# Kernel tuning notes

Hardware: AMD Instinct MI355X
Metric: run time of the kernel (lower is better)

Reference implementation:

```python
import jax, jax.numpy as jnp
import numpy as np

N_NODES = 50000
IN, H, OUT = 128, 256, 128  # in_channels, hidden_channels, out_channels
E, PE = 640000, 500000
EPS = 1e-5


def setup_inputs() -> dict:
    key = jax.random.key(0)
    ks = jax.random.split(key, 12)
    def rn(k, shape, s=0.05):
        return jax.random.normal(k, shape, jnp.float32) * s
    return {
        "x": jax.random.normal(ks[0], (N_NODES, IN), jnp.float32),
        "edge_index": jax.random.randint(ks[1], (2, E), 0, N_NODES, jnp.int32),
        "pred_edge_index": jax.random.randint(ks[2], (2, PE), 0, N_NODES, jnp.int32),
        # SAGEConv 1: out = mean_neighbors @ W_l^T + x @ W_r^T + b (PyG default, root_weight=True)
        "W1l": rn(ks[3], (H, IN)), "W1r": rn(ks[4], (H, IN)), "b1": jnp.zeros((H,), jnp.float32),
        "bn1_g": jnp.ones((H,), jnp.float32), "bn1_b": jnp.zeros((H,), jnp.float32),
        "bn1_m": jnp.zeros((H,), jnp.float32), "bn1_v": jnp.ones((H,), jnp.float32),
        # SAGEConv 2
        "W2l": rn(ks[5], (OUT, H)), "W2r": rn(ks[6], (OUT, H)), "b2": jnp.zeros((OUT,), jnp.float32),
        # LinkPredictor MLP
        "pW1": rn(ks[7], (H, 2 * OUT)), "pb1": jnp.zeros((H,), jnp.float32),
        "pbn1_g": jnp.ones((H,), jnp.float32), "pbn1_b": jnp.zeros((H,), jnp.float32),
        "pbn1_m": jnp.zeros((H,), jnp.float32), "pbn1_v": jnp.ones((H,), jnp.float32),
        "pW2": rn(ks[8], (H // 2, H)), "pb2": jnp.zeros((H // 2,), jnp.float32),
        "pbn2_g": jnp.ones((H // 2,), jnp.float32), "pbn2_b": jnp.zeros((H // 2,), jnp.float32),
        "pbn2_m": jnp.zeros((H // 2,), jnp.float32), "pbn2_v": jnp.ones((H // 2,), jnp.float32),
        "pW3": rn(ks[9], (1, H // 2)), "pb3": jnp.zeros((1,), jnp.float32),
    }


def _bn(x, g, b, m, v):
    # BatchNorm1d in eval mode (running stats)
    return (x - m) * jax.lax.rsqrt(v + EPS) * g + b


def _sage(x, src, dst, Wl, Wr, b):
    # mean aggregation of source features onto targets (gather-scatter)
    agg = jax.ops.segment_sum(x[src], dst, num_segments=N_NODES)
    cnt = jax.ops.segment_sum(jnp.ones(src.shape, x.dtype), dst, num_segments=N_NODES)
    mean = agg / jnp.maximum(cnt, 1.0)[:, None]
    return mean @ Wl.T + x @ Wr.T + b


def reference(x, edge_index, pred_edge_index, W1l, W1r, b1, bn1_g, bn1_b, bn1_m, bn1_v,
              W2l, W2r, b2, pW1, pb1, pbn1_g, pbn1_b, pbn1_m, pbn1_v,
              pW2, pb2, pbn2_g, pbn2_b, pbn2_m, pbn2_v, pW3, pb3):
    src, dst = edge_index[0], edge_index[1]
    # encoder (dropout is identity in eval mode)
    h = _sage(x, src, dst, W1l, W1r, b1)
    h = jax.nn.relu(_bn(h, bn1_g, bn1_b, bn1_m, bn1_v))
    z = _sage(h, src, dst, W2l, W2r, b2)  # [N_NODES, OUT]
    # decoder: gather endpoint embeddings and run MLP
    q = jnp.concatenate([z[pred_edge_index[0]], z[pred_edge_index[1]]], axis=-1)  # [PE, 2*OUT]
    q = jax.nn.relu(_bn(q @ pW1.T + pb1, pbn1_g, pbn1_b, pbn1_m, pbn1_v))
    q = jax.nn.relu(_bn(q @ pW2.T + pb2, pbn2_g, pbn2_b, pbn2_m, pbn2_v))
    return (q @ pW3.T + pb3).squeeze(-1)  # [PE]
```

## Files before the change

kernel.cpp:

```cpp
#include <hip/hip_runtime.h>
#include <hip/hip_bf16.h>

#define NN   50000
#define NE   640000
#define NPE  500000
#define FEPS 1e-5f

typedef __attribute__((ext_vector_type(8))) short          bf16x8;
typedef __attribute__((ext_vector_type(8))) unsigned short u16x8;
typedef __attribute__((ext_vector_type(4))) float          f32x4;

__device__ inline float b2f(unsigned short u) {
    union { unsigned int i; float f; } c; c.i = (unsigned int)u << 16; return c.f;
}
__device__ inline unsigned short f2b(float f) {
    __hip_bfloat16 h = __float2bfloat16(f);
    return *reinterpret_cast<unsigned short*>(&h);
}

__global__ __launch_bounds__(256) void k_init(
    int4* __restrict__ zdst,
    const float* __restrict__ x, unsigned short* __restrict__ xbf,
    const float* __restrict__ W1l, const float* __restrict__ W1r,
    const float* __restrict__ W2l, const float* __restrict__ W2r,
    const float* __restrict__ pW1, const float* __restrict__ pW2,
    unsigned short* __restrict__ wdst) {
    int b = blockIdx.x, t = threadIdx.x;
    if (b < 196) {
        int i = b * 256 + t;
        if (i < 50048) zdst[i] = make_int4(0, 0, 0, 0);
        return;
    }
    const float* src;
    size_t off;
    if (b < 3321) {
        int i = (b - 196) * 256 + t;
        if (i >= 800000) return;
        const float4* p = (const float4*)x + 2 * (size_t)i;
        float4 a = p[0], c = p[1];
        u16x8 o;
        o[0]=f2b(a.x); o[1]=f2b(a.y); o[2]=f2b(a.z); o[3]=f2b(a.w);
        o[4]=f2b(c.x); o[5]=f2b(c.y); o[6]=f2b(c.z); o[7]=f2b(c.w);
        *((u16x8*)xbf + i) = o;
        return;
    }
    int i = (b - 3321) * 256 + t;
    if (i >= 28672) return;
    if      (i < 4096)  { src = W1l; off = i; }
    else if (i < 8192)  { src = W1r; off = i - 4096; }
    else if (i < 12288) { src = W2l; off = i - 8192; }
    else if (i < 16384) { src = W2r; off = i - 12288; }
    else if (i < 24576) { src = pW1; off = i - 16384; }
    else                { src = pW2; off = i - 24576; }
    const float4* p = (const float4*)src + 2 * off;
    float4 a = p[0], c = p[1];
    u16x8 o;
    o[0]=f2b(a.x); o[1]=f2b(a.y); o[2]=f2b(a.z); o[3]=f2b(a.w);
    o[4]=f2b(c.x); o[5]=f2b(c.y); o[6]=f2b(c.z); o[7]=f2b(c.w);
    *((u16x8*)wdst + i) = o;
}

__global__ void k_hist(const int* __restrict__ key, int* __restrict__ cnt, int n) {
    int e = blockIdx.x * blockDim.x + threadIdx.x;
    if (e < n) atomicAdd(&cnt[key[e]], 1);
}

__global__ void k_scan1(const int* __restrict__ cnt, int* __restrict__ part) {
    int t = threadIdx.x, lane = t & 63, w = t >> 6;
    int i = blockIdx.x * 256 + t;
    int v = (i < NN) ? cnt[i] : 0;
#pragma unroll
    for (int d = 1; d < 64; d <<= 1) v += __shfl_xor(v, d, 64);
    __shared__ int ws[4];
    if (lane == 0) ws[w] = v;
    __syncthreads();
    if (t == 0) part[blockIdx.x] = ws[0] + ws[1] + ws[2] + ws[3];
}

__global__ void k_scan2(int* __restrict__ part) {
    int t = threadIdx.x, lane = t & 63, w = t >> 6;
    int v = (t < 196) ? part[t] : 0;
    int s = v;
#pragma unroll
    for (int d = 1; d < 64; d <<= 1) { int u = __shfl_up(s, d, 64); if (lane >= d) s += u; }
    __shared__ int ws[4];
    if (lane == 63) ws[w] = s;
    __syncthreads();
    if (t == 0) { int a = 0; for (int k = 0; k < 4; ++k) { int tmp = ws[k]; ws[k] = a; a += tmp; } }
    __syncthreads();
    if (t < 196) part[t] = ws[w] + s - v;
}

__global__ void k_scan3(const int* __restrict__ cnt, const int* __restrict__ part,
                        int* __restrict__ rowptr) {
    int t = threadIdx.x, lane = t & 63, w = t >> 6;
    int i = blockIdx.x * 256 + t;
    int v = (i < NN) ? cnt[i] : 0;
    int s = v;
#pragma unroll
    for (int d = 1; d < 64; d <<= 1) { int u = __shfl_up(s, d, 64); if (lane >= d) s += u; }
    __shared__ int ws[4];
    if (lane == 63) ws[w] = s;
    __syncthreads();
    if (t == 0) { int a = 0; for (int k = 0; k < 4; ++k) { int tmp = ws[k]; ws[k] = a; a += tmp; } }
    __syncthreads();
    if (i <= NN) rowptr[i] = part[blockIdx.x] + ws[w] + s - v;
}

__global__ void k_fill(const int* __restrict__ src, const int* __restrict__ dst,
                       const int* __restrict__ rowptr, int* __restrict__ cursor,
                       int* __restrict__ col) {
    int e = blockIdx.x * blockDim.x + threadIdx.x;
    if (e >= NE) return;
    int d = dst[e];
    int slot = atomicAdd(&cursor[d], 1);
    col[rowptr[d] + slot] = src[e];
}

__global__ void k_fill2(const int* __restrict__ pu, const int* __restrict__ pv,
                        const int* __restrict__ rowptr2, int* __restrict__ cursor2,
                        int* __restrict__ su, int2* __restrict__ svi) {
    int e = blockIdx.x * blockDim.x + threadIdx.x;
    if (e >= NPE) return;
    int u = pu[e];
    int slot = atomicAdd(&cursor2[u], 1);
    int pos = rowptr2[u] + slot;
    su[pos] = u;
    svi[pos] = make_int2(pv[e], e);
}

__global__ __launch_bounds__(256) void k_mean(const unsigned short* __restrict__ feat,
                                              const int* __restrict__ rowptr,
                                              const int* __restrict__ col,
                                              unsigned short* __restrict__ outm) {
    int node = blockIdx.x * 4 + (threadIdx.x >> 6);
    int lane = threadIdx.x & 63;
    if (node >= NN) return;
    int beg = rowptr[node], end = rowptr[node + 1];
    float a0 = 0.f, a1 = 0.f;
    int j = beg;
    for (; j + 8 <= end; j += 8) {
        int s[8];
#pragma unroll
        for (int k = 0; k < 8; ++k) s[k] = col[j + k];
        unsigned int v[8];
#pragma unroll
        for (int k = 0; k < 8; ++k)
            v[k] = *(const unsigned int*)(feat + (size_t)s[k] * 128 + lane * 2);
#pragma unroll
        for (int k = 0; k < 8; ++k) { a0 += b2f(v[k] & 0xffff); a1 += b2f(v[k] >> 16); }
    }
    if (j + 4 <= end) {
        int s[4];
#pragma unroll
        for (int k = 0; k < 4; ++k) s[k] = col[j + k];
        unsigned int v[4];
#pragma unroll
        for (int k = 0; k < 4; ++k)
            v[k] = *(const unsigned int*)(feat + (size_t)s[k] * 128 + lane * 2);
#pragma unroll
        for (int k = 0; k < 4; ++k) { a0 += b2f(v[k] & 0xffff); a1 += b2f(v[k] >> 16); }
        j += 4;
    }
    for (; j < end; ++j) {
        int s = col[j];
        unsigned int v = *(const unsigned int*)(feat + (size_t)s * 128 + lane * 2);
        a0 += b2f(v & 0xffff); a1 += b2f(v >> 16);
    }
    float inv = 1.f / fmaxf((float)(end - beg), 1.f);
    unsigned int v = (unsigned int)f2b(a0 * inv) | ((unsigned int)f2b(a1 * inv) << 16);
    *(unsigned int*)(outm + (size_t)node * 128 + lane * 2) = v;
}

__global__ __launch_bounds__(256) void k_sage12(
    const unsigned short* __restrict__ mean, const unsigned short* __restrict__ self,
    const unsigned short* __restrict__ Wl, const unsigned short* __restrict__ Wr,
    const float* __restrict__ b, const float* __restrict__ bg, const float* __restrict__ bb,
    const float* __restrict__ bm, const float* __restrict__ bv,
    const unsigned short* __restrict__ W2l, const unsigned short* __restrict__ W2r,
    const float* __restrict__ b2,
    unsigned short* __restrict__ Y, unsigned short* __restrict__ S) {
    __shared__ unsigned short AB[64 * 256];
    unsigned short* ms = AB;
    unsigned short* xs = AB + 64 * 128;
    int t = threadIdx.x;
    int n0 = blockIdx.x * 64;
    for (int j = 0; j < 4; ++j) {
        int idx = t + j * 256;
        int row = idx >> 4, c16 = idx & 15;
        int node = n0 + row;
        u16x8 v = {0,0,0,0,0,0,0,0}, v2 = {0,0,0,0,0,0,0,0};
        if (node < NN) {
            v  = *(const u16x8*)(mean + (size_t)node * 128 + c16 * 8);
            v2 = *(const u16x8*)(self + (size_t)node * 128 + c16 * 8);
        }
        int byte = row * 256 + ((c16 * 16) ^ ((row & 7) << 4));
        *(u16x8*)((char*)ms + byte) = v;
        *(u16x8*)((char*)xs + byte) = v2;
    }
    __syncthreads();
    int w = t >> 6, l = t & 63, lr = l & 15, lh = l >> 4;
    f32x4 acc[4][4];
#pragma unroll
    for (int mi = 0; mi < 4; ++mi)
#pragma unroll
        for (int ni = 0; ni < 4; ++ni) { acc[mi][ni][0]=0; acc[mi][ni][1]=0; acc[mi][ni][2]=0; acc[mi][ni][3]=0; }
#pragma unroll
    for (int half = 0; half < 2; ++half) {
        const unsigned short* A = half ? xs : ms;
        const unsigned short* W = half ? Wr : Wl;
#pragma unroll
        for (int ks = 0; ks < 4; ++ks) {
            int k0 = ks * 32;
            bf16x8 a[4], wf[4];
#pragma unroll
            for (int mi = 0; mi < 4; ++mi) {
                int row = mi * 16 + lr;
                int byte = row * 256 + ((k0 * 2 + lh * 16) ^ ((row & 7) << 4));
                a[mi] = *(const bf16x8*)((const char*)A + byte);
            }
#pragma unroll
            for (int ni = 0; ni < 4; ++ni) {
                int wrow = w * 64 + ni * 16 + lr;
                wf[ni] = *(const bf16x8*)(W + (size_t)wrow * 128 + k0 + lh * 8);
            }
#pragma unroll
            for (int mi = 0; mi < 4; ++mi)
#pragma unroll
                for (int ni = 0; ni < 4; ++ni)
                    acc[mi][ni] = __builtin_amdgcn_mfma_f32_16x16x32_bf16(a[mi], wf[ni], acc[mi][ni], 0, 0, 0);
        }
    }
    __syncthreads();
#pragma unroll
    for (int ni = 0; ni < 4; ++ni) {
        int ch = w * 64 + ni * 16 + lr;
        float sc = bg[ch] * rsqrtf(bv[ch] + FEPS);
        float sh = bb[ch] - bm[ch] * sc;
        float bias = b[ch];
#pragma unroll
        for (int mi = 0; mi < 4; ++mi)
#pragma unroll
            for (int r = 0; r < 4; ++r) {
                int row = mi * 16 + lh * 4 + r;
                float vv = fmaxf((acc[mi][ni][r] + bias) * sc + sh, 0.f);
                int byte = row * 512 + ((ch * 2) ^ ((row & 7) << 4));
                *(unsigned short*)((char*)AB + byte) = f2b(vv);
            }
    }
    __syncthreads();
    f32x4 aY[4][2], aS[4][2];
#pragma unroll
    for (int mi = 0; mi < 4; ++mi)
#pragma unroll
        for (int ni = 0; ni < 2; ++ni) {
            aY[mi][ni][0]=0; aY[mi][ni][1]=0; aY[mi][ni][2]=0; aY[mi][ni][3]=0;
            aS[mi][ni][0]=0; aS[mi][ni][1]=0; aS[mi][ni][2]=0; aS[mi][ni][3]=0;
        }
#pragma unroll
    for (int ks = 0; ks < 8; ++ks) {
        int k0 = ks * 32;
        bf16x8 a[4], wl[2], wr[2];
#pragma unroll
        for (int mi = 0; mi < 4; ++mi) {
            int row = mi * 16 + lr;
            int byte = row * 512 + ((k0 * 2 + lh * 16) ^ ((row & 7) << 4));
            a[mi] = *(const bf16x8*)((const char*)AB + byte);
        }
#pragma unroll
        for (int ni = 0; ni < 2; ++ni) {
            int wrow = w * 32 + ni * 16 + lr;
            wl[ni] = *(const bf16x8*)(W2l + (size_t)wrow * 256 + k0 + lh * 8);
            wr[ni] = *(const bf16x8*)(W2r + (size_t)wrow * 256 + k0 + lh * 8);
        }
#pragma unroll
        for (int mi = 0; mi < 4; ++mi)
#pragma unroll
            for (int ni = 0; ni < 2; ++ni) {
                aY[mi][ni] = __builtin_amdgcn_mfma_f32_16x16x32_bf16(a[mi], wl[ni], aY[mi][ni], 0, 0, 0);
                aS[mi][ni] = __builtin_amdgcn_mfma_f32_16x16x32_bf16(a[mi], wr[ni], aS[mi][ni], 0, 0, 0);
            }
    }
#pragma unroll
    for (int ni = 0; ni < 2; ++ni) {
        int ch = w * 32 + ni * 16 + lr;
        float bias = b2[ch];
#pragma unroll
        for (int mi = 0; mi < 4; ++mi)
#pragma unroll
            for (int r = 0; r < 4; ++r) {
                int node = n0 + mi * 16 + lh * 4 + r;
                if (node < NN) {
                    Y[(size_t)node * 128 + ch] = f2b(aY[mi][ni][r]);
                    S[(size_t)node * 128 + ch] = f2b(aS[mi][ni][r] + bias);
                }
            }
    }
}

__global__ __launch_bounds__(256) void k_prep(
    const unsigned short* __restrict__ S,
    const unsigned short* __restrict__ mY,
    const unsigned short* __restrict__ W1,
    const float* __restrict__ b1, const float* __restrict__ g1,
    const float* __restrict__ be1, const float* __restrict__ m1, const float* __restrict__ v1,
    unsigned short* __restrict__ Pa, unsigned short* __restrict__ Pb) {
    __shared__ unsigned short zs[64 * 128];
    int t = threadIdx.x;
    int tile = blockIdx.x >> 1, side = blockIdx.x & 1;
    int n0 = tile * 64;
    for (int j = 0; j < 4; ++j) {
        int idx = t + j * 256;
        int row = idx >> 4, c16 = idx & 15;
        int node = n0 + row;
        u16x8 o = {0,0,0,0,0,0,0,0};
        if (node < NN) {
            u16x8 sv = *(const u16x8*)(S  + (size_t)node * 128 + c16 * 8);
            u16x8 mv = *(const u16x8*)(mY + (size_t)node * 128 + c16 * 8);
#pragma unroll
            for (int jj = 0; jj < 8; ++jj)
                o[jj] = f2b(b2f((unsigned short)sv[jj]) + b2f((unsigned short)mv[jj]));
        }
        int byte = row * 256 + ((c16 * 16) ^ ((row & 7) << 4));
        *(u16x8*)((char*)zs + byte) = o;
    }
    __syncthreads();
    int w = t >> 6, l = t & 63, lr = l & 15, lh = l >> 4;
    f32x4 acc[4][4];
#pragma unroll
    for (int mi = 0; mi < 4; ++mi)
#pragma unroll
        for (int ni = 0; ni < 4; ++ni) { acc[mi][ni][0]=0; acc[mi][ni][1]=0; acc[mi][ni][2]=0; acc[mi][ni][3]=0; }
#pragma unroll
    for (int ks = 0; ks < 4; ++ks) {
        int k0 = ks * 32;
        bf16x8 a[4], wf[4];
#pragma unroll
        for (int mi = 0; mi < 4; ++mi) {
            int row = mi * 16 + lr;
            int byte = row * 256 + ((k0 * 2 + lh * 16) ^ ((row & 7) << 4));
            a[mi] = *(const bf16x8*)((const char*)zs + byte);
        }
#pragma unroll
        for (int ni = 0; ni < 4; ++ni) {
            int ch = w * 64 + ni * 16 + lr;
            wf[ni] = *(const bf16x8*)(W1 + (size_t)ch * 256 + side * 128 + k0 + lh * 8);
        }
#pragma unroll
        for (int mi = 0; mi < 4; ++mi)
#pragma unroll
            for (int ni = 0; ni < 4; ++ni)
                acc[mi][ni] = __builtin_amdgcn_mfma_f32_16x16x32_bf16(a[mi], wf[ni], acc[mi][ni], 0, 0, 0);
    }
    unsigned short* P = side ? Pb : Pa;
#pragma unroll
    for (int ni = 0; ni < 4; ++ni) {
        int ch = w * 64 + ni * 16 + lr;
        float sc = g1[ch] * rsqrtf(v1[ch] + FEPS);
        float add = side ? 0.f : ((b1[ch] - m1[ch]) * sc + be1[ch]);
#pragma unroll
        for (int mi = 0; mi < 4; ++mi)
#pragma unroll
            for (int r = 0; r < 4; ++r) {
                int node = n0 + mi * 16 + lh * 4 + r;
                if (node < NN)
                    P[(size_t)node * 256 + ch] = f2b(acc[mi][ni][r] * sc + add);
            }
    }
}

__global__ __launch_bounds__(256, 5) void k_mlp(
    const unsigned short* __restrict__ Pa, const unsigned short* __restrict__ Pb,
    const int* __restrict__ su, const int2* __restrict__ svi,
    const unsigned short* __restrict__ W2, const float* __restrict__ b2,
    const float* __restrict__ g2, const float* __restrict__ be2,
    const float* __restrict__ m2, const float* __restrict__ v2,
    const float* __restrict__ W3, const float* __restrict__ b3,
    float* __restrict__ out) {
    __shared__ unsigned short q1[64 * 256];
    int t = threadIdx.x;
    const int q = 976, r = 5;
    int bid = blockIdx.x;
    int xcd = bid & 7, ii = bid >> 3;
    int wg = (xcd < r) ? (xcd * (q + 1) + ii) : (r * (q + 1) + (xcd - r) * q + ii);
    int e0 = wg * 64;
#pragma unroll
    for (int batch = 0; batch < 2; ++batch) {
        u16x8 A[4], B[4];
        int bofs[4];
#pragma unroll
        for (int j = 0; j < 4; ++j) {
            int idx = t + (batch * 4 + j) * 256;
            int edge = idx >> 5, c16 = idx & 31;
            int ge = e0 + edge;
            if (ge < NPE) {
                int u = su[ge];
                int2 vi = svi[ge];
                A[j] = *(const u16x8*)(Pa + (size_t)u    * 256 + c16 * 8);
                B[j] = *(const u16x8*)(Pb + (size_t)vi.x * 256 + c16 * 8);
            } else {
                A[j] = (u16x8){0,0,0,0,0,0,0,0};
                B[j] = (u16x8){0,0,0,0,0,0,0,0};
            }
            bofs[j] = edge * 512 + ((c16 * 16) ^ ((edge & 7) << 4));
        }
#pragma unroll
        for (int j = 0; j < 4; ++j) {
            u16x8 o;
#pragma unroll
            for (int jj = 0; jj < 8; ++jj)
                o[jj] = f2b(fmaxf(b2f((unsigned short)A[j][jj]) + b2f((unsigned short)B[j][jj]), 0.f));
            *(u16x8*)((char*)q1 + bofs[j]) = o;
        }
    }
    __syncthreads();
    int w = t >> 6, l = t & 63, lr = l & 15, lh = l >> 4;
    f32x4 acc[4][2];
#pragma unroll
    for (int mi = 0; mi < 4; ++mi)
#pragma unroll
        for (int ni = 0; ni < 2; ++ni) { acc[mi][ni][0]=0; acc[mi][ni][1]=0; acc[mi][ni][2]=0; acc[mi][ni][3]=0; }
#pragma unroll
    for (int ks = 0; ks < 8; ++ks) {
        int k0 = ks * 32;
        bf16x8 a[4], wf[2];
#pragma unroll
        for (int mi = 0; mi < 4; ++mi) {
            int row = mi * 16 + lr;
            int byte = row * 512 + ((k0 * 2 + lh * 16) ^ ((row & 7) << 4));
            a[mi] = *(const bf16x8*)((const char*)q1 + byte);
        }
#pragma unroll
        for (int ni = 0; ni < 2; ++ni) {
            int wrow = w * 32 + ni * 16 + lr;
            wf[ni] = *(const bf16x8*)(W2 + (size_t)wrow * 256 + k0 + lh * 8);
        }
#pragma unroll
        for (int mi = 0; mi < 4; ++mi)
#pragma unroll
            for (int ni = 0; ni < 2; ++ni)
                acc[mi][ni] = __builtin_amdgcn_mfma_f32_16x16x32_bf16(a[mi], wf[ni], acc[mi][ni], 0, 0, 0);
    }
    __syncthreads();
#pragma unroll
    for (int ni = 0; ni < 2; ++ni) {
        int ch = w * 32 + ni * 16 + lr;
        float sc = g2[ch] * rsqrtf(v2[ch] + FEPS);
        float sh = be2[ch] - m2[ch] * sc;
        float bias = b2[ch];
#pragma unroll
        for (int mi = 0; mi < 4; ++mi)
#pragma unroll
            for (int r = 0; r < 4; ++r) {
                int row = mi * 16 + lh * 4 + r;
                float vv = fmaxf((acc[mi][ni][r] + bias) * sc + sh, 0.f);
                int byte = row * 256 + ((ch * 2) ^ ((row & 7) << 4));
                *(unsigned short*)((char*)q1 + byte) = f2b(vv);
            }
    }
    __syncthreads();
    {
        int edge = t >> 2, part = t & 3;
        float p = 0.f;
#pragma unroll
        for (int s = 0; s < 4; ++s) {
            int byte = edge * 256 + ((part * 64 + s * 16) ^ ((edge & 7) << 4));
            u16x8 v = *(const u16x8*)((const char*)q1 + byte);
#pragma unroll
            for (int jj = 0; jj < 8; ++jj)
                p += b2f((unsigned short)v[jj]) * W3[part * 32 + s * 8 + jj];
        }
        p += __shfl_xor(p, 1, 64);
        p += __shfl_xor(p, 2, 64);
        int ge = e0 + edge;
        if (part == 0 && ge < NPE) out[svi[ge].y] = p + b3[0];
    }
}

extern "C" void kernel_launch(void* const* d_in, const int* in_sizes, int n_in,
                              void* d_out, int out_size, void* d_ws, size_t ws_size,
                              hipStream_t stream) {
    const float* x    = (const float*)d_in[0];
    const int*   ei   = (const int*)d_in[1];
    const int*   pei  = (const int*)d_in[2];
    const float* W1l  = (const float*)d_in[3];
    const float* W1r  = (const float*)d_in[4];
    const float* b1   = (const float*)d_in[5];
    const float* bn1g = (const float*)d_in[6];
    const float* bn1b = (const float*)d_in[7];
    const float* bn1m = (const float*)d_in[8];
    const float* bn1v = (const float*)d_in[9];
    const float* W2l  = (const float*)d_in[10];
    const float* W2r  = (const float*)d_in[11];
    const float* b2   = (const float*)d_in[12];
    const float* pW1  = (const float*)d_in[13];
    const float* pb1  = (const float*)d_in[14];
    const float* pg1  = (const float*)d_in[15];
    const float* pbb1 = (const float*)d_in[16];
    const float* pm1  = (const float*)d_in[17];
    const float* pv1  = (const float*)d_in[18];
    const float* pW2  = (const float*)d_in[19];
    const float* pb2  = (const float*)d_in[20];
    const float* pg2  = (const float*)d_in[21];
    const float* pbb2 = (const float*)d_in[22];
    const float* pm2  = (const float*)d_in[23];
    const float* pv2  = (const float*)d_in[24];
    const float* pW3  = (const float*)d_in[25];
    const float* pb3  = (const float*)d_in[26];
    float* out = (float*)d_out;

    const int* src = ei;
    const int* dst = ei + NE;
    const int* pu  = pei;
    const int* pv  = pei + NPE;

    char* p = (char*)d_ws;
    auto alloc = [&](size_t bytes) -> char* {
        char* r = p; p += (bytes + 255) & ~(size_t)255; return r;
    };
    int* cnt     = (int*)alloc((size_t)NN * 4);
    int* cursor  = (int*)alloc((size_t)NN * 4);
    int* cnt2    = (int*)alloc((size_t)NN * 4);
    int* cursor2 = (int*)alloc((size_t)NN * 4);
    int* part    = (int*)alloc(256 * 4);
    int* part2   = (int*)alloc(256 * 4);
    int* rowptr  = (int*)alloc((size_t)(NN + 1) * 4);
    int* rowptr2 = (int*)alloc((size_t)(NN + 1) * 4);
    int* col     = (int*)alloc((size_t)NE * 4);
    int* su      = (int*)alloc((size_t)NPE * 4);
    int2* svi    = (int2*)alloc((size_t)NPE * 8);
    unsigned short* xbf  = (unsigned short*)alloc((size_t)NN * 128 * 2);
    unsigned short* mx   = (unsigned short*)alloc((size_t)NN * 128 * 2);
    unsigned short* Ybf  = (unsigned short*)alloc((size_t)NN * 128 * 2);
    unsigned short* mY   = (unsigned short*)alloc((size_t)NN * 128 * 2);
    unsigned short* Sbf  = (unsigned short*)alloc((size_t)NN * 128 * 2);
    unsigned short* Pa   = (unsigned short*)alloc((size_t)NN * 256 * 2);
    unsigned short* W1lb = (unsigned short*)alloc((size_t)256 * 128 * 2);
    unsigned short* W1rb = (unsigned short*)alloc((size_t)256 * 128 * 2);
    unsigned short* W2lb = (unsigned short*)alloc((size_t)128 * 256 * 2);
    unsigned short* W2rb = (unsigned short*)alloc((size_t)128 * 256 * 2);
    unsigned short* pW1b = (unsigned short*)alloc((size_t)256 * 256 * 2);
    unsigned short* pW2b = (unsigned short*)alloc((size_t)128 * 256 * 2);
    unsigned short* Pb = xbf;

    k_init<<<3433, 256, 0, stream>>>((int4*)cnt, x, xbf,
                                     W1l, W1r, W2l, W2r, pW1, pW2, W1lb);
    k_hist<<<2500, 256, 0, stream>>>(dst, cnt, NE);
    k_scan1<<<196, 256, 0, stream>>>(cnt, part);
    k_scan2<<<1, 256, 0, stream>>>(part);
    k_scan3<<<196, 256, 0, stream>>>(cnt, part, rowptr);
    k_fill<<<2500, 256, 0, stream>>>(src, dst, rowptr, cursor, col);
    k_hist<<<1954, 256, 0, stream>>>(pu, cnt2, NPE);
    k_scan1<<<196, 256, 0, stream>>>(cnt2, part2);
    k_scan2<<<1, 256, 0, stream>>>(part2);
    k_scan3<<<196, 256, 0, stream>>>(cnt2, part2, rowptr2);
    k_fill2<<<1954, 256, 0, stream>>>(pu, pv, rowptr2, cursor2, su, svi);

    k_mean<<<12500, 256, 0, stream>>>(xbf, rowptr, col, mx);
    k_sage12<<<782, 256, 0, stream>>>(mx, xbf, W1lb, W1rb, b1, bn1g, bn1b, bn1m, bn1v,
                                      W2lb, W2rb, b2, Ybf, Sbf);
    k_mean<<<12500, 256, 0, stream>>>(Ybf, rowptr, col, mY);

    k_prep<<<1564, 256, 0, stream>>>(Sbf, mY, pW1b, pb1, pg1, pbb1, pm1, pv1, Pa, Pb);

    k_mlp<<<(NPE + 63) / 64, 256, 0, stream>>>(Pa, Pb, su, svi,
                                               pW2b, pb2, pg2, pbb2, pm2, pv2,
                                               pW3, pb3, out);
}
```

Measured before the change: 418.1 us.

## Drop pred-edge CSR sort, vectorize mean gather, fuse prep sides per tile

Removes the second histogram, scan and fill pass that sorted prediction edges by source node, so the MLP now reads pu/pv directly and writes output in original order. This gives up source locality in the Pa gathers in exchange for skipping five kernel launches and their atomics. The mean aggregation now has each wave gather four neighbours at once with 16-byte loads per lane, then reduces across the four lane groups with shuffles. k_prep computes both sides in one block, so the staged tile is loaded once instead of twice. The init kernel zeroes only the counters that are still used.

```diff
diff --git a/kernel.cpp b/kernel.cpp
--- a/kernel.cpp
+++ b/kernel.cpp
@@ -26,15 +26,15 @@
     const float* __restrict__ pW1, const float* __restrict__ pW2,
     unsigned short* __restrict__ wdst) {
     int b = blockIdx.x, t = threadIdx.x;
-    if (b < 196) {
+    if (b < 98) {
         int i = b * 256 + t;
-        if (i < 50048) zdst[i] = make_int4(0, 0, 0, 0);
+        if (i < 25088) zdst[i] = make_int4(0, 0, 0, 0);
         return;
     }
     const float* src;
     size_t off;
-    if (b < 3321) {
-        int i = (b - 196) * 256 + t;
+    if (b < 3223) {
+        int i = (b - 98) * 256 + t;
         if (i >= 800000) return;
         const float4* p = (const float4*)x + 2 * (size_t)i;
         float4 a = p[0], c = p[1];
@@ -44,7 +44,7 @@
         *((u16x8*)xbf + i) = o;
         return;
     }
-    int i = (b - 3321) * 256 + t;
+    int i = (b - 3223) * 256 + t;
     if (i >= 28672) return;
     if      (i < 4096)  { src = W1l; off = i; }
     else if (i < 8192)  { src = W1r; off = i - 4096; }
@@ -117,59 +117,49 @@
     col[rowptr[d] + slot] = src[e];
 }
 
-__global__ void k_fill2(const int* __restrict__ pu, const int* __restrict__ pv,
-                        const int* __restrict__ rowptr2, int* __restrict__ cursor2,
-                        int* __restrict__ su, int2* __restrict__ svi) {
-    int e = blockIdx.x * blockDim.x + threadIdx.x;
-    if (e >= NPE) return;
-    int u = pu[e];
-    int slot = atomicAdd(&cursor2[u], 1);
-    int pos = rowptr2[u] + slot;
-    su[pos] = u;
-    svi[pos] = make_int2(pv[e], e);
-}
-
 __global__ __launch_bounds__(256) void k_mean(const unsigned short* __restrict__ feat,
                                               const int* __restrict__ rowptr,
                                               const int* __restrict__ col,
                                               unsigned short* __restrict__ outm) {
     int node = blockIdx.x * 4 + (threadIdx.x >> 6);
     int lane = threadIdx.x & 63;
+    int g = lane >> 4, li = lane & 15;
     if (node >= NN) return;
     int beg = rowptr[node], end = rowptr[node + 1];
-    float a0 = 0.f, a1 = 0.f;
+    float acc[8];
+#pragma unroll
+    for (int k = 0; k < 8; ++k) acc[k] = 0.f;
     int j = beg;
     for (; j + 8 <= end; j += 8) {
-        int s[8];
-#pragma unroll
-        for (int k = 0; k < 8; ++k) s[k] = col[j + k];
-        unsigned int v[8];
+        int s0 = col[j + g], s1 = col[j + 4 + g];
+        u16x8 v0 = *(const u16x8*)(feat + (size_t)s0 * 128 + li * 8);
+        u16x8 v1 = *(const u16x8*)(feat + (size_t)s1 * 128 + li * 8);
 #pragma unroll
         for (int k = 0; k < 8; ++k)
-            v[k] = *(const unsigned int*)(feat + (size_t)s[k] * 128 + lane * 2);
-#pragma unroll
-        for (int k = 0; k < 8; ++k) { a0 += b2f(v[k] & 0xffff); a1 += b2f(v[k] >> 16); }
-    }
-    if (j + 4 <= end) {
-        int s[4];
-#pragma unroll
-        for (int k = 0; k < 4; ++k) s[k] = col[j + k];
-        unsigned int v[4];
-#pragma unroll
-        for (int k = 0; k < 4; ++k)
-            v[k] = *(const unsigned int*)(feat + (size_t)s[k] * 128 + lane * 2);
-#pragma unroll
-        for (int k = 0; k < 4; ++k) { a0 += b2f(v[k] & 0xffff); a1 += b2f(v[k] >> 16); }
-        j += 4;
-    }
-    for (; j < end; ++j) {
-        int s = col[j];
-        unsigned int v = *(const unsigned int*)(feat + (size_t)s * 128 + lane * 2);
-        a0 += b2f(v & 0xffff); a1 += b2f(v >> 16);
-    }
-    float inv = 1.f / fmaxf((float)(end - beg), 1.f);
-    unsigned int v = (unsigned int)f2b(a0 * inv) | ((unsigned int)f2b(a1 * inv) << 16);
-    *(unsigned int*)(outm + (size_t)node * 128 + lane * 2) = v;
+            acc[k] += b2f((unsigned short)v0[k]) + b2f((unsigned short)v1[k]);
+    }
+    for (; j < end; j += 4) {
+        int idx = j + g;
+        bool ok = idx < end;
+        int s = ok ? col[idx] : col[beg];
+        u16x8 v = *(const u16x8*)(feat + (size_t)s * 128 + li * 8);
+        if (ok) {
+#pragma unroll
+            for (int k = 0; k < 8; ++k) acc[k] += b2f((unsigned short)v[k]);
+        }
+    }
+#pragma unroll
+    for (int k = 0; k < 8; ++k) {
+        acc[k] += __shfl_xor(acc[k], 16, 64);
+        acc[k] += __shfl_xor(acc[k], 32, 64);
+    }
+    if (g == 0) {
+        float inv = 1.f / fmaxf((float)(end - beg), 1.f);
+        u16x8 o;
+#pragma unroll
+        for (int k = 0; k < 8; ++k) o[k] = f2b(acc[k] * inv);
+        *(u16x8*)(outm + (size_t)node * 128 + li * 8) = o;
+    }
 }
 
 __global__ __launch_bounds__(256) void k_sage12(
@@ -307,8 +297,7 @@
     unsigned short* __restrict__ Pa, unsigned short* __restrict__ Pb) {
     __shared__ unsigned short zs[64 * 128];
     int t = threadIdx.x;
-    int tile = blockIdx.x >> 1, side = blockIdx.x & 1;
-    int n0 = tile * 64;
+    int n0 = blockIdx.x * 64;
     for (int j = 0; j < 4; ++j) {
         int idx = t + j * 256;
         int row = idx >> 4, c16 = idx & 15;
@@ -326,52 +315,55 @@
     }
     __syncthreads();
     int w = t >> 6, l = t & 63, lr = l & 15, lh = l >> 4;
-    f32x4 acc[4][4];
-#pragma unroll
-    for (int mi = 0; mi < 4; ++mi)
-#pragma unroll
-        for (int ni = 0; ni < 4; ++ni) { acc[mi][ni][0]=0; acc[mi][ni][1]=0; acc[mi][ni][2]=0; acc[mi][ni][3]=0; }
-#pragma unroll
-    for (int ks = 0; ks < 4; ++ks) {
-        int k0 = ks * 32;
-        bf16x8 a[4], wf[4];
-#pragma unroll
-        for (int mi = 0; mi < 4; ++mi) {
-            int row = mi * 16 + lr;
-            int byte = row * 256 + ((k0 * 2 + lh * 16) ^ ((row & 7) << 4));
-            a[mi] = *(const bf16x8*)((const char*)zs + byte);
-        }
+#pragma unroll
+    for (int side = 0; side < 2; ++side) {
+        f32x4 acc[4][4];
+#pragma unroll
+        for (int mi = 0; mi < 4; ++mi)
+#pragma unroll
+            for (int ni = 0; ni < 4; ++ni) { acc[mi][ni][0]=0; acc[mi][ni][1]=0; acc[mi][ni][2]=0; acc[mi][ni][3]=0; }
+#pragma unroll
+        for (int ks = 0; ks < 4; ++ks) {
+            int k0 = ks * 32;
+            bf16x8 a[4], wf[4];
+#pragma unroll
+            for (int mi = 0; mi < 4; ++mi) {
+                int row = mi * 16 + lr;
+                int byte = row * 256 + ((k0 * 2 + lh * 16) ^ ((row & 7) << 4));
+                a[mi] = *(const bf16x8*)((const char*)zs + byte);
+            }
+#pragma unroll
+            for (int ni = 0; ni < 4; ++ni) {
+                int ch = w * 64 + ni * 16 + lr;
+                wf[ni] = *(const bf16x8*)(W1 + (size_t)ch * 256 + side * 128 + k0 + lh * 8);
+            }
+#pragma unroll
+            for (int mi = 0; mi < 4; ++mi)
+#pragma unroll
+                for (int ni = 0; ni < 4; ++ni)
+                    acc[mi][ni] = __builtin_amdgcn_mfma_f32_16x16x32_bf16(a[mi], wf[ni], acc[mi][ni], 0, 0, 0);
+        }
+        unsigned short* P = side ? Pb : Pa;
 #pragma unroll
         for (int ni = 0; ni < 4; ++ni) {
             int ch = w * 64 + ni * 16 + lr;
-            wf[ni] = *(const bf16x8*)(W1 + (size_t)ch * 256 + side * 128 + k0 + lh * 8);
-        }
-#pragma unroll
-        for (int mi = 0; mi < 4; ++mi)
-#pragma unroll
-            for (int ni = 0; ni < 4; ++ni)
-                acc[mi][ni] = __builtin_amdgcn_mfma_f32_16x16x32_bf16(a[mi], wf[ni], acc[mi][ni], 0, 0, 0);
-    }
-    unsigned short* P = side ? Pb : Pa;
-#pragma unroll
-    for (int ni = 0; ni < 4; ++ni) {
-        int ch = w * 64 + ni * 16 + lr;
-        float sc = g1[ch] * rsqrtf(v1[ch] + FEPS);
-        float add = side ? 0.f : ((b1[ch] - m1[ch]) * sc + be1[ch]);
-#pragma unroll
-        for (int mi = 0; mi < 4; ++mi)
-#pragma unroll
-            for (int r = 0; r < 4; ++r) {
-                int node = n0 + mi * 16 + lh * 4 + r;
-                if (node < NN)
-                    P[(size_t)node * 256 + ch] = f2b(acc[mi][ni][r] * sc + add);
-            }
+            float sc = g1[ch] * rsqrtf(v1[ch] + FEPS);
+            float add = side ? 0.f : ((b1[ch] - m1[ch]) * sc + be1[ch]);
+#pragma unroll
+            for (int mi = 0; mi < 4; ++mi)
+#pragma unroll
+                for (int r = 0; r < 4; ++r) {
+                    int node = n0 + mi * 16 + lh * 4 + r;
+                    if (node < NN)
+                        P[(size_t)node * 256 + ch] = f2b(acc[mi][ni][r] * sc + add);
+                }
+        }
     }
 }
 
 __global__ __launch_bounds__(256, 5) void k_mlp(
     const unsigned short* __restrict__ Pa, const unsigned short* __restrict__ Pb,
-    const int* __restrict__ su, const int2* __restrict__ svi,
+    const int* __restrict__ pu, const int* __restrict__ pv,
     const unsigned short* __restrict__ W2, const float* __restrict__ b2,
     const float* __restrict__ g2, const float* __restrict__ be2,
     const float* __restrict__ m2, const float* __restrict__ v2,
@@ -379,11 +371,7 @@
     float* __restrict__ out) {
     __shared__ unsigned short q1[64 * 256];
     int t = threadIdx.x;
-    const int q = 976, r = 5;
-    int bid = blockIdx.x;
-    int xcd = bid & 7, ii = bid >> 3;
-    int wg = (xcd < r) ? (xcd * (q + 1) + ii) : (r * (q + 1) + (xcd - r) * q + ii);
-    int e0 = wg * 64;
+    int e0 = blockIdx.x * 64;
 #pragma unroll
     for (int batch = 0; batch < 2; ++batch) {
         u16x8 A[4], B[4];
@@ -394,10 +382,9 @@
             int edge = idx >> 5, c16 = idx & 31;
             int ge = e0 + edge;
             if (ge < NPE) {
-                int u = su[ge];
-                int2 vi = svi[ge];
-                A[j] = *(const u16x8*)(Pa + (size_t)u    * 256 + c16 * 8);
-                B[j] = *(const u16x8*)(Pb + (size_t)vi.x * 256 + c16 * 8);
+                int u = pu[ge], vv = pv[ge];
+                A[j] = *(const u16x8*)(Pa + (size_t)u  * 256 + c16 * 8);
+                B[j] = *(const u16x8*)(Pb + (size_t)vv * 256 + c16 * 8);
             } else {
                 A[j] = (u16x8){0,0,0,0,0,0,0,0};
                 B[j] = (u16x8){0,0,0,0,0,0,0,0};
@@ -473,7 +460,7 @@
         p += __shfl_xor(p, 1, 64);
         p += __shfl_xor(p, 2, 64);
         int ge = e0 + edge;
-        if (part == 0 && ge < NPE) out[svi[ge].y] = p + b3[0];
+        if (part == 0 && ge < NPE) out[ge] = p + b3[0];
     }
 }
 
@@ -520,15 +507,9 @@
     };
     int* cnt     = (int*)alloc((size_t)NN * 4);
     int* cursor  = (int*)alloc((size_t)NN * 4);
-    int* cnt2    = (int*)alloc((size_t)NN * 4);
-    int* cursor2 = (int*)alloc((size_t)NN * 4);
     int* part    = (int*)alloc(256 * 4);
-    int* part2   = (int*)alloc(256 * 4);
     int* rowptr  = (int*)alloc((size_t)(NN + 1) * 4);
-    int* rowptr2 = (int*)alloc((size_t)(NN + 1) * 4);
     int* col     = (int*)alloc((size_t)NE * 4);
-    int* su      = (int*)alloc((size_t)NPE * 4);
-    int2* svi    = (int2*)alloc((size_t)NPE * 8);
     unsigned short* xbf  = (unsigned short*)alloc((size_t)NN * 128 * 2);
     unsigned short* mx   = (unsigned short*)alloc((size_t)NN * 128 * 2);
     unsigned short* Ybf  = (unsigned short*)alloc((size_t)NN * 128 * 2);
@@ -543,27 +524,22 @@
     unsigned short* pW2b = (unsigned short*)alloc((size_t)128 * 256 * 2);
     unsigned short* Pb = xbf;
 
-    k_init<<<3433, 256, 0, stream>>>((int4*)cnt, x, xbf,
+    k_init<<<3335, 256, 0, stream>>>((int4*)cnt, x, xbf,
                                      W1l, W1r, W2l, W2r, pW1, pW2, W1lb);
     k_hist<<<2500, 256, 0, stream>>>(dst, cnt, NE);
     k_scan1<<<196, 256, 0, stream>>>(cnt, part);
     k_scan2<<<1, 256, 0, stream>>>(part);
     k_scan3<<<196, 256, 0, stream>>>(cnt, part, rowptr);
     k_fill<<<2500, 256, 0, stream>>>(src, dst, rowptr, cursor, col);
-    k_hist<<<1954, 256, 0, stream>>>(pu, cnt2, NPE);
-    k_scan1<<<196, 256, 0, stream>>>(cnt2, part2);
-    k_scan2<<<1, 256, 0, stream>>>(part2);
-    k_scan3<<<196, 256, 0, stream>>>(cnt2, part2, rowptr2);
-    k_fill2<<<1954, 256, 0, stream>>>(pu, pv, rowptr2, cursor2, su, svi);
 
     k_mean<<<12500, 256, 0, stream>>>(xbf, rowptr, col, mx);
     k_sage12<<<782, 256, 0, stream>>>(mx, xbf, W1lb, W1rb, b1, bn1g, bn1b, bn1m, bn1v,
                                       W2lb, W2rb, b2, Ybf, Sbf);
     k_mean<<<12500, 256, 0, stream>>>(Ybf, rowptr, col, mY);
 
-    k_prep<<<1564, 256, 0, stream>>>(Sbf, mY, pW1b, pb1, pg1, pbb1, pm1, pv1, Pa, Pb);
-
-    k_mlp<<<(NPE + 63) / 64, 256, 0, stream>>>(Pa, Pb, su, svi,
+    k_prep<<<782, 256, 0, stream>>>(Sbf, mY, pW1b, pb1, pg1, pbb1, pm1, pv1, Pa, Pb);
+
+    k_mlp<<<(NPE + 63) / 64, 256, 0, stream>>>(Pa, Pb, pu, pv,
                                                pW2b, pb2, pg2, pbb2, pm2, pv2,
                                                pW3, pb3, out);
 }
```

Result: faster. 346.8 us (-17.1%).
